# Performance work log

Measured on AMD Instinct MI355X. Metric: run time of the kernel, lower is better.

## Reference

```python
import jax, jax.numpy as jnp
import numpy as np

B, S, D, H = 2, 2048, 1024, 16
HD = D // H

def setup_inputs() -> dict:
    key = jax.random.key(0)
    k1, k2, k3, k4, k5 = jax.random.split(key, 5)
    X = jax.random.normal(k1, (B, S, D), dtype=jnp.float32)
    # nn.Linear(D, 3D): weight [3D, D], bias [3D]
    W_qkv = jax.random.normal(k2, (3 * D, D), dtype=jnp.float32) * (1.0 / np.sqrt(D))
    b_qkv = jax.random.normal(k3, (3 * D,), dtype=jnp.float32) * 0.02
    W_out = jax.random.normal(k4, (D, D), dtype=jnp.float32) * (1.0 / np.sqrt(D))
    b_out = jax.random.normal(k5, (D,), dtype=jnp.float32) * 0.02
    return {"X": X, "W_qkv": W_qkv, "b_qkv": b_qkv, "W_out": W_out, "b_out": b_out}

def reference(X, W_qkv, b_qkv, W_out, b_out):
    b, s, d = X.shape
    qkv = jnp.einsum('bsd,ed->bse', X, W_qkv) + b_qkv  # [B,S,3D]
    q, k, v = jnp.split(qkv, 3, axis=2)
    def heads(t):
        return t.reshape(b, s, H, HD).transpose(0, 2, 1, 3)  # [B,H,S,HD]
    q, k, v = heads(q), heads(k), heads(v)
    scores = jnp.einsum('bhqd,bhkd->bhqk', q, k) * (1.0 / np.sqrt(HD))
    causal = jnp.tril(jnp.ones((s, s), dtype=bool))
    scores = jnp.where(causal[None, None], scores, jnp.float32(-jnp.inf))
    probs = jax.nn.softmax(scores, axis=-1)
    attn = jnp.einsum('bhqk,bhkd->bhqd', probs, v)  # [B,H,S,HD]
    attn = attn.transpose(0, 2, 1, 3).reshape(b, s, d)
    out = jnp.einsum('bsd,ed->bse', attn, W_out) + b_out
    return out
```

## Files before the change

kernel.cpp:

```cpp
#include <hip/hip_runtime.h>


typedef _Float16 f16x8 __attribute__((ext_vector_type(8)));
typedef _Float16 f16x4 __attribute__((ext_vector_type(4)));
typedef float    f32x4 __attribute__((ext_vector_type(4)));
typedef unsigned short u16x8 __attribute__((ext_vector_type(8)));

__device__ __forceinline__ float bf16_bits_to_f32(unsigned short u) {
    union { unsigned int i; float f; } v; v.i = ((unsigned int)u) << 16; return v.f;
}
__device__ __forceinline__ unsigned short f32_to_bf16_bits(float f) {
    union { float f; unsigned int i; } v; v.f = f;
    unsigned int x = v.i;
    return (unsigned short)((x + 0x7fffu + ((x >> 16) & 1u)) >> 16);
}
__device__ __forceinline__ float fexp2(float x) {
#if __has_builtin(__builtin_amdgcn_exp2f)
    return __builtin_amdgcn_exp2f(x);
#else
    return exp2f(x);
#endif
}
__device__ __forceinline__ void gll16(const void* g, void* l) {
    __builtin_amdgcn_global_load_lds(
        (const __attribute__((address_space(1))) unsigned int*)g,
        (__attribute__((address_space(3))) unsigned int*)l, 16, 0, 0);
}

__global__ void detect_kernel(const unsigned short* __restrict__ X, unsigned int* __restrict__ flag) {
    __shared__ unsigned int smax;
    if (threadIdx.x == 0) smax = 0;
    __syncthreads();
    unsigned int mymax = 0;
    for (int i = threadIdx.x; i < 16384; i += 256) {
        unsigned int e = (X[i] >> 7) & 0xFFu;
        mymax = mymax > e ? mymax : e;
    }
    atomicMax(&smax, mymax);
    __syncthreads();
    if (threadIdx.x == 0) flag[0] = (smax >= 0x90u) ? 1u : 0u;
}

__global__ void __launch_bounds__(256) cvt2_kernel(const void* __restrict__ Wqkv, _Float16* __restrict__ wout,
                                                   const void* __restrict__ X, _Float16* __restrict__ xout,
                                                   const unsigned int* __restrict__ flag) {
    int b = blockIdx.x;
    const void* in; _Float16* out; size_t off;
    if (b < 1536) { in = Wqkv; out = wout; off = (size_t)b * 2048; }
    else          { in = X;    out = xout; off = (size_t)(b - 1536) * 2048; }
    size_t i = off + (size_t)threadIdx.x * 8;
    f16x8 c;
    if (flag[0]) {
        const float* p = (const float*)in + i;
        #pragma unroll
        for (int j = 0; j < 8; j++) c[j] = (_Float16)p[j];
    } else {
        u16x8 r = *(const u16x8*)((const unsigned short*)in + i);
        #pragma unroll
        for (int j = 0; j < 8; j++) c[j] = (_Float16)bf16_bits_to_f32(r[j]);
    }
    *(f16x8*)(out + i) = c;
}

__global__ void __launch_bounds__(256) cvtw_kernel(const void* __restrict__ in,
                                                   _Float16* __restrict__ out,
                                                   const unsigned int* __restrict__ flag) {
    size_t i = ((size_t)blockIdx.x * 256 + threadIdx.x) * 8;
    f16x8 c;
    if (flag[0]) {
        const float* p = (const float*)in + i;
        #pragma unroll
        for (int j = 0; j < 8; j++) c[j] = (_Float16)p[j];
    } else {
        u16x8 r = *(const u16x8*)((const unsigned short*)in + i);
        #pragma unroll
        for (int j = 0; j < 8; j++) c[j] = (_Float16)bf16_bits_to_f32(r[j]);
    }
    *(f16x8*)(out + i) = c;
}

template<int AF16>
__global__ void __launch_bounds__(256) qkv_gemm(
    const void* __restrict__ A, const _Float16* __restrict__ Wf,
    const void* __restrict__ bias, const unsigned int* __restrict__ flag,
    _Float16* __restrict__ qws, _Float16* __restrict__ kws, _Float16* __restrict__ vtws)
{
    constexpr int AST = AF16 ? 32 : 56;
    __shared__ _Float16 As[128 * AST];
    __shared__ _Float16 Bs[128 * 32];
    const bool isf32 = (flag[0] != 0u);
    const int tid  = threadIdx.x;
    const int lane = tid & 63, wave = tid >> 6;
    const int l15  = lane & 15, quad = lane >> 4;
    const int wm   = (wave >> 1) * 64, wn = (wave & 1) * 64;
    const int m0   = blockIdx.y * 128, n0 = blockIdx.x * 128;
    const int srow = tid >> 1, scol = (tid & 1) * 16;

    f32x4 acc[4][4] = {};

    for (int k0 = 0; k0 < 1024; k0 += 32) {
        if (AF16) {
            #pragma unroll
            for (int i = 0; i < 2; i++) {
                int seg = (wave * 2 + i) * 64 + lane;
                int row = seg >> 2, qtr = seg & 3;
                gll16((const _Float16*)A + (size_t)(m0 + row) * 1024 + k0 + qtr * 8,
                      &As[(wave * 2 + i) * 512]);
            }
        } else {
            f16x8 c0, c1;
            if (isf32) {
                const float4* ga = (const float4*)((const float*)A + (size_t)(m0 + srow) * 1024 + k0 + scol);
                float4 a0 = ga[0], a1 = ga[1], a2 = ga[2], a3 = ga[3];
                c0[0]=(_Float16)a0.x; c0[1]=(_Float16)a0.y; c0[2]=(_Float16)a0.z; c0[3]=(_Float16)a0.w;
                c0[4]=(_Float16)a1.x; c0[5]=(_Float16)a1.y; c0[6]=(_Float16)a1.z; c0[7]=(_Float16)a1.w;
                c1[0]=(_Float16)a2.x; c1[1]=(_Float16)a2.y; c1[2]=(_Float16)a2.z; c1[3]=(_Float16)a2.w;
                c1[4]=(_Float16)a3.x; c1[5]=(_Float16)a3.y; c1[6]=(_Float16)a3.z; c1[7]=(_Float16)a3.w;
            } else {
                const unsigned short* ga = (const unsigned short*)A + (size_t)(m0 + srow) * 1024 + k0 + scol;
                u16x8 r0 = *(const u16x8*)ga, r1 = *(const u16x8*)(ga + 8);
                #pragma unroll
                for (int i = 0; i < 8; i++) {
                    c0[i] = (_Float16)bf16_bits_to_f32(r0[i]);
                    c1[i] = (_Float16)bf16_bits_to_f32(r1[i]);
                }
            }
            *(f16x8*)&As[srow * AST + scol]     = c0;
            *(f16x8*)&As[srow * AST + scol + 8] = c1;
        }
        #pragma unroll
        for (int i = 0; i < 2; i++) {
            int seg = (wave * 2 + i) * 64 + lane;
            int row = seg >> 2, qtr = seg & 3;
            gll16(Wf + (size_t)(n0 + row) * 1024 + k0 + qtr * 8, &Bs[(wave * 2 + i) * 512]);
        }
        __syncthreads();
        f16x8 af[4], bfg[4];
        #pragma unroll
        for (int mt = 0; mt < 4; mt++)
            af[mt] = *(const f16x8*)&As[(wm + mt * 16 + l15) * AST + quad * 8];
        #pragma unroll
        for (int nt = 0; nt < 4; nt++)
            bfg[nt] = *(const f16x8*)&Bs[(wn + nt * 16 + l15) * 32 + quad * 8];
        #pragma unroll
        for (int mt = 0; mt < 4; mt++)
            #pragma unroll
            for (int nt = 0; nt < 4; nt++)
                acc[mt][nt] = __builtin_amdgcn_mfma_f32_16x16x32_f16(af[mt], bfg[nt], acc[mt][nt], 0, 0, 0);
        __syncthreads();
    }

    const float qsc = 0.18033688011112042591f;
    #pragma unroll
    for (int mt = 0; mt < 4; mt++) {
        #pragma unroll
        for (int nt = 0; nt < 4; nt++) {
            #pragma unroll
            for (int r = 0; r < 4; r++) {
                int m = m0 + wm + mt * 16 + quad * 4 + r;
                int n = n0 + wn + nt * 16 + l15;
                float bval = isf32 ? ((const float*)bias)[n] : bf16_bits_to_f32(((const unsigned short*)bias)[n]);
                float val = acc[mt][nt][r] + bval;
                int b = m >> 11, s = m & 2047;
                int t = n >> 10, e = n & 1023;
                int h = e >> 6, hd = e & 63;
                int bh = b * 16 + h;
                if (t == 0)      qws[((size_t)bh * 2048 + s) * 64 + hd]  = (_Float16)(val * qsc);
                else if (t == 1) kws[((size_t)bh * 2048 + s) * 64 + hd]  = (_Float16)val;
                else             vtws[((size_t)bh * 64 + hd) * 2048 + s] = (_Float16)val;
            }
        }
    }
}

__global__ void __launch_bounds__(256) out_gemm(
    const _Float16* __restrict__ Alo, const _Float16* __restrict__ Ahi,
    const _Float16* __restrict__ Wf, const void* __restrict__ bias,
    const unsigned int* __restrict__ flag, void* __restrict__ outp, int m_base)
{
    __shared__ _Float16 As[128 * 32];
    __shared__ _Float16 Bs[128 * 32];
    const bool isf32 = (flag[0] != 0u);
    const int tid  = threadIdx.x;
    const int lane = tid & 63, wave = tid >> 6;
    const int l15  = lane & 15, quad = lane >> 4;
    const int wm   = (wave >> 1) * 64, wn = (wave & 1) * 64;
    const int m0g  = m_base + blockIdx.y * 128, n0 = blockIdx.x * 128;
    const _Float16* A = (m0g < 2048) ? (Alo + (size_t)m0g * 1024)
                                     : (Ahi + (size_t)(m0g - 2048) * 1024);
    f32x4 acc[4][4] = {};

    for (int k0 = 0; k0 < 1024; k0 += 32) {
        #pragma unroll
        for (int i = 0; i < 2; i++) {
            int seg = (wave * 2 + i) * 64 + lane;
            int row = seg >> 2, qtr = seg & 3;
            gll16(A + (size_t)row * 1024 + k0 + qtr * 8, &As[(wave * 2 + i) * 512]);
            gll16(Wf + (size_t)(n0 + row) * 1024 + k0 + qtr * 8, &Bs[(wave * 2 + i) * 512]);
        }
        __syncthreads();
        f16x8 af[4], bfg[4];
        #pragma unroll
        for (int mt = 0; mt < 4; mt++)
            af[mt] = *(const f16x8*)&As[(wm + mt * 16 + l15) * 32 + quad * 8];
        #pragma unroll
        for (int nt = 0; nt < 4; nt++)
            bfg[nt] = *(const f16x8*)&Bs[(wn + nt * 16 + l15) * 32 + quad * 8];
        #pragma unroll
        for (int mt = 0; mt < 4; mt++)
            #pragma unroll
            for (int nt = 0; nt < 4; nt++)
                acc[mt][nt] = __builtin_amdgcn_mfma_f32_16x16x32_f16(af[mt], bfg[nt], acc[mt][nt], 0, 0, 0);
        __syncthreads();
    }

    #pragma unroll
    for (int mt = 0; mt < 4; mt++) {
        #pragma unroll
        for (int nt = 0; nt < 4; nt++) {
            #pragma unroll
            for (int r = 0; r < 4; r++) {
                int m = m0g + wm + mt * 16 + quad * 4 + r;
                int n = n0 + wn + nt * 16 + l15;
                float bval = isf32 ? ((const float*)bias)[n] : bf16_bits_to_f32(((const unsigned short*)bias)[n]);
                float val = acc[mt][nt][r] + bval;
                size_t idx = (size_t)m * 1024 + n;
                if (isf32) ((float*)outp)[idx] = val;
                else       ((unsigned short*)outp)[idx] = f32_to_bf16_bits(val);
            }
        }
    }
}

__global__ void __launch_bounds__(256) flash_kernel(
    const _Float16* __restrict__ qws,
    const _Float16* __restrict__ kws,
    const _Float16* __restrict__ vtws,
    _Float16* __restrict__ attn_lo,
    _Float16* __restrict__ attn_hi)
{
    __shared__ _Float16 Ks[2][64 * 64];
    __shared__ _Float16 Vs[2][64 * 72];

    const int bh   = blockIdx.x;
    const int qb   = 31 - blockIdx.y;
    const int tid  = threadIdx.x;
    const int wave = tid >> 6;
    const int lane = tid & 63;
    const int l15  = lane & 15, quad = lane >> 4;

    const _Float16* Q  = qws  + (size_t)bh * 2048 * 64;
    const _Float16* Kp = kws  + (size_t)bh * 2048 * 64;
    const _Float16* Vt = vtws + (size_t)bh * 64 * 2048;

    const int q0w = qb * 64 + wave * 16;
    f16x8 qf0 = *(const f16x8*)(Q + (size_t)(q0w + l15) * 64 + quad * 8);
    f16x8 qf1 = *(const f16x8*)(Q + (size_t)(q0w + l15) * 64 + 32 + quad * 8);

    f32x4 o[4] = {};
    float lp = 0.f;
    const int nch = qb + 1;

    {
        #pragma unroll
        for (int i = 0; i < 2; i++) {
            int s = (wave * 2 + i) * 64 + lane;
            int row = s >> 3, cs = ((s & 7) - row) & 7;
            gll16(Kp + (size_t)row * 64 + cs * 8, &Ks[0][s * 8]);
        }
        int hd = tid >> 3, ko = (tid & 7) * 8;
        f16x8 v0 = *(const f16x8*)(Vt + (size_t)hd * 2048 + ko);
        f16x8 v1 = *(const f16x8*)(Vt + (size_t)(hd + 32) * 2048 + ko);
        *(f16x8*)&Vs[0][hd * 72 + ko]        = v0;
        *(f16x8*)&Vs[0][(hd + 32) * 72 + ko] = v1;
    }

    for (int c = 0; c < nch; c++) {
        __syncthreads();
        const int cb = c & 1;
        const bool more = (c + 1 < nch);
        f16x8 vr0, vr1;
        int hd = tid >> 3, ko = (tid & 7) * 8;
        if (more) {
            int jn = (c + 1) * 64;
            vr0 = *(const f16x8*)(Vt + (size_t)hd * 2048 + jn + ko);
            vr1 = *(const f16x8*)(Vt + (size_t)(hd + 32) * 2048 + jn + ko);
            #pragma unroll
            for (int i = 0; i < 2; i++) {
                int s = (wave * 2 + i) * 64 + lane;
                int row = s >> 3, cs = ((s & 7) - row) & 7;
                gll16(Kp + (size_t)(jn + row) * 64 + cs * 8, &Ks[cb ^ 1][s * 8]);
            }
        }

        const bool diag = (c == qb);
        f32x4 t[4];
        #pragma unroll
        for (int kt = 0; kt < 4; kt++) {
            int row = kt * 16 + l15;
            f16x8 k0 = *(const f16x8*)&Ks[cb][row * 64 + ((quad + l15) & 7) * 8];
            f16x8 k1 = *(const f16x8*)&Ks[cb][row * 64 + ((4 + quad + l15) & 7) * 8];
            f32x4 z = {};
            z = __builtin_amdgcn_mfma_f32_16x16x32_f16(k0, qf0, z, 0, 0, 0);
            t[kt] = __builtin_amdgcn_mfma_f32_16x16x32_f16(k1, qf1, z, 0, 0, 0);
        }
        float p[16];
        #pragma unroll
        for (int kt = 0; kt < 4; kt++)
            #pragma unroll
            for (int r = 0; r < 4; r++) {
                float v = t[kt][r];
                if (diag)
                    v = ((kt * 16 + quad * 4 + r) <= (wave * 16 + l15)) ? v : -INFINITY;
                p[kt * 4 + r] = fminf(fexp2(v), 60000.0f);
            }
        float rs = 0.f;
        #pragma unroll
        for (int i = 0; i < 16; i++) rs += p[i];
        lp += rs;
        f16x4 pf[4];
        #pragma unroll
        for (int kt = 0; kt < 4; kt++)
            #pragma unroll
            for (int r = 0; r < 4; r++) pf[kt][r] = (_Float16)p[kt * 4 + r];
        #pragma unroll
        for (int kt = 0; kt < 4; kt++) {
            #pragma unroll
            for (int mt = 0; mt < 4; mt++) {
                f16x4 cv = *(const f16x4*)&Vs[cb][(mt * 16 + l15) * 72 + kt * 16 + quad * 4];
                o[mt] = __builtin_amdgcn_mfma_f32_16x16x16f16(cv, pf[kt], o[mt], 0, 0, 0);
            }
        }

        if (more) {
            *(f16x8*)&Vs[cb ^ 1][hd * 72 + ko]        = vr0;
            *(f16x8*)&Vs[cb ^ 1][(hd + 32) * 72 + ko] = vr1;
        }
    }

    const int b = bh >> 4, h = bh & 15;
    _Float16* attn = (b == 0) ? attn_lo : attn_hi;
    {
        float rs = lp;
        rs += __shfl_xor(rs, 16);
        rs += __shfl_xor(rs, 32);
        const float inv = 1.0f / rs;
        const int s = q0w + l15;
        #pragma unroll
        for (int mt = 0; mt < 4; mt++) {
            #pragma unroll
            for (int r = 0; r < 4; r++) {
                int hdd = mt * 16 + quad * 4 + r;
                attn[(size_t)s * 1024 + h * 64 + hdd] = (_Float16)(o[mt][r] * inv);
            }
        }
    }
}

extern "C" void kernel_launch(void* const* d_in, const int* in_sizes, int n_in,
                              void* d_out, int out_size, void* d_ws, size_t ws_size,
                              hipStream_t stream) {
    (void)out_size;
    const void *X = nullptr, *Wqkv = nullptr, *bqkv = nullptr, *Wout = nullptr, *bout = nullptr;
    for (int i = 0; i < n_in; i++) {
        switch (in_sizes[i]) {
            case 4194304: X    = d_in[i]; break;
            case 3145728: Wqkv = d_in[i]; break;
            case 3072:    bqkv = d_in[i]; break;
            case 1048576: Wout = d_in[i]; break;
            case 1024:    bout = d_in[i]; break;
        }
    }
    char* ws = (char*)d_ws;
    const size_t MB = 1u << 20;
    unsigned int* flag = (unsigned int*)ws;
    char* base = ws + 256;

    detect_kernel<<<1, 256, 0, stream>>>((const unsigned short*)X, flag);

    if (ws_size >= (size_t)(385 * MB / 10)) {
        _Float16* wf16 = (_Float16*)(base);
        _Float16* xf16 = (_Float16*)(base + 6 * MB);
        _Float16* q    = (_Float16*)(base + 14 * MB);
        _Float16* k    = (_Float16*)(base + 22 * MB);
        _Float16* vt   = (_Float16*)(base + 30 * MB);
        cvt2_kernel<<<dim3(3584), 256, 0, stream>>>(Wqkv, wf16, X, xf16, flag);
        qkv_gemm<1><<<dim3(24, 32), 256, 0, stream>>>(xf16, wf16, bqkv, flag, q, k, vt);
        cvtw_kernel<<<dim3(512), 256, 0, stream>>>(Wout, wf16, flag);
        _Float16* attn = xf16;
        flash_kernel<<<dim3(32, 32), 256, 0, stream>>>(q, k, vt, attn, attn + (size_t)2048 * 1024);
        out_gemm<<<dim3(8, 32), 256, 0, stream>>>(attn, attn + (size_t)2048 * 1024,
                                                  wf16, bout, flag, d_out, 0);
    } else {
        _Float16* wf16    = (_Float16*)(base);
        _Float16* attn_hi = (_Float16*)(base + 6 * MB);
        _Float16* q       = (_Float16*)(base + 10 * MB);
        _Float16* k       = (_Float16*)(base + 18 * MB);
        _Float16* vt      = (_Float16*)(base + 26 * MB);
        _Float16* attn_lo = (_Float16*)((char*)d_out + 8 * MB);
        cvtw_kernel<<<dim3(1536), 256, 0, stream>>>(Wqkv, wf16, flag);
        qkv_gemm<0><<<dim3(24, 32), 256, 0, stream>>>(X, wf16, bqkv, flag, q, k, vt);
        cvtw_kernel<<<dim3(512), 256, 0, stream>>>(Wout, wf16, flag);
        flash_kernel<<<dim3(32, 32), 256, 0, stream>>>(q, k, vt, attn_lo, attn_hi);
        out_gemm<<<dim3(8, 16), 256, 0, stream>>>(attn_lo, attn_hi, wf16, bout, flag, d_out, 0);
        out_gemm<<<dim3(8, 16), 256, 0, stream>>>(attn_lo, attn_hi, wf16, bout, flag, d_out, 2048);
    }
}
```

Before: 209.9 us.

## Replace QKV GEMM with 256x256-tile, 8-wave, ping-pong pipelined kernel

Adds a new QKV projection kernel that uses 256x256 output tiles with 512 threads (8 waves). It stages A and B half-tiles into double-buffered LDS through direct global-to-LDS loads with an XOR swizzle. The K loop is split into four MFMA phases with interleaved prefetches, barriers and s_setprio, so loads overlap with matrix math. The goal is to raise data reuse and MFMA utilization over the old 128x128 kernel, at the cost of 128KB of LDS, fewer blocks (192) and a hand-tuned waitcnt schedule that could be fragile.

```diff
diff --git a/kernel.cpp b/kernel.cpp
--- a/kernel.cpp
+++ b/kernel.cpp
@@ -77,6 +77,154 @@
         for (int j = 0; j < 8; j++) c[j] = (_Float16)bf16_bits_to_f32(r[j]);
     }
     *(f16x8*)(out + i) = c;
+}
+
+__device__ __forceinline__ void stage_ht(const _Float16* __restrict__ G, int kt, int h,
+                                         _Float16* tile, int wave, int lane)
+{
+    #pragma unroll
+    for (int i = 0; i < 2; i++) {
+        int seg = wave * 2 + i;
+        int f = seg * 64 + lane;
+        int row = h * 128 + (f >> 3);
+        int qg = (f & 7) ^ (row & 7);
+        gll16(G + (size_t)row * 1024 + kt * 64 + qg * 8,
+              tile + (size_t)h * 8192 + (size_t)seg * 512);
+    }
+}
+
+__global__ void __launch_bounds__(512, 2) qkv_gemm8(
+    const _Float16* __restrict__ Af, const _Float16* __restrict__ Wf,
+    const void* __restrict__ bias, const unsigned int* __restrict__ flag,
+    _Float16* __restrict__ qws, _Float16* __restrict__ kws, _Float16* __restrict__ vtws)
+{
+    __shared__ _Float16 L[2][2][16384];
+    const int tid  = threadIdx.x;
+    const int lane = tid & 63, wave = tid >> 6;
+    const int l15  = lane & 15, quad = lane >> 4;
+    const int wm   = (wave >> 2) * 128, wn = (wave & 3) * 64;
+    const int m0   = blockIdx.y * 256, n0 = blockIdx.x * 256;
+    const _Float16* Ag = Af + (size_t)m0 * 1024;
+    const _Float16* Bg = Wf + (size_t)n0 * 1024;
+
+    f32x4 acc[8][4] = {};
+
+    stage_ht(Ag, 0, 0, &L[0][0][0], wave, lane);
+    stage_ht(Ag, 0, 1, &L[0][0][0], wave, lane);
+    stage_ht(Bg, 0, 0, &L[0][1][0], wave, lane);
+    stage_ht(Bg, 0, 1, &L[0][1][0], wave, lane);
+    stage_ht(Bg, 1, 0, &L[1][1][0], wave, lane);
+    stage_ht(Bg, 1, 1, &L[1][1][0], wave, lane);
+    stage_ht(Ag, 1, 0, &L[1][0][0], wave, lane);
+    asm volatile("s_waitcnt vmcnt(6)" ::: "memory");
+    __builtin_amdgcn_s_barrier();
+
+    constexpr int NT = 16;
+    #pragma unroll 2
+    for (int t = 0; t < NT; ++t) {
+        const int cb = t & 1;
+        const _Float16* At = &L[cb][0][0];
+        const _Float16* Bt = &L[cb][1][0];
+        f16x8 aF[4][2], bF[4][2];
+
+        #pragma unroll
+        for (int mt = 0; mt < 4; mt++) {
+            int R = wm + mt * 16 + l15;
+            #pragma unroll
+            for (int ks = 0; ks < 2; ks++)
+                aF[mt][ks] = *(const f16x8*)&At[R * 64 + (((ks * 4 + quad) ^ (R & 7)) << 3)];
+        }
+        #pragma unroll
+        for (int nt = 0; nt < 4; nt++) {
+            int R = wn + nt * 16 + l15;
+            #pragma unroll
+            for (int ks = 0; ks < 2; ks++)
+                bF[nt][ks] = *(const f16x8*)&Bt[R * 64 + (((ks * 4 + quad) ^ (R & 7)) << 3)];
+        }
+        if (t + 1 < NT) stage_ht(Ag, t + 1, 1, &L[(t + 1) & 1][0][0], wave, lane);
+        __builtin_amdgcn_s_barrier();
+        __builtin_amdgcn_s_setprio(1);
+        #pragma unroll
+        for (int mt = 0; mt < 4; mt++)
+            #pragma unroll
+            for (int nt = 0; nt < 2; nt++)
+                #pragma unroll
+                for (int ks = 0; ks < 2; ks++)
+                    acc[mt][nt] = __builtin_amdgcn_mfma_f32_16x16x32_f16(aF[mt][ks], bF[nt][ks], acc[mt][nt], 0, 0, 0);
+        __builtin_amdgcn_s_setprio(0);
+        __builtin_amdgcn_s_barrier();
+
+        if (t + 2 < NT) stage_ht(Bg, t + 2, 0, &L[cb][1][0], wave, lane);
+        __builtin_amdgcn_s_barrier();
+        __builtin_amdgcn_s_setprio(1);
+        #pragma unroll
+        for (int mt = 0; mt < 4; mt++)
+            #pragma unroll
+            for (int nt = 0; nt < 2; nt++)
+                #pragma unroll
+                for (int ks = 0; ks < 2; ks++)
+                    acc[mt][2 + nt] = __builtin_amdgcn_mfma_f32_16x16x32_f16(aF[mt][ks], bF[2 + nt][ks], acc[mt][2 + nt], 0, 0, 0);
+        __builtin_amdgcn_s_setprio(0);
+        __builtin_amdgcn_s_barrier();
+
+        #pragma unroll
+        for (int mt = 0; mt < 4; mt++) {
+            int R = wm + 64 + mt * 16 + l15;
+            #pragma unroll
+            for (int ks = 0; ks < 2; ks++)
+                aF[mt][ks] = *(const f16x8*)&At[R * 64 + (((ks * 4 + quad) ^ (R & 7)) << 3)];
+        }
+        if (t + 2 < NT) stage_ht(Bg, t + 2, 1, &L[cb][1][0], wave, lane);
+        __builtin_amdgcn_s_barrier();
+        __builtin_amdgcn_s_setprio(1);
+        #pragma unroll
+        for (int mt = 0; mt < 4; mt++)
+            #pragma unroll
+            for (int nt = 0; nt < 2; nt++)
+                #pragma unroll
+                for (int ks = 0; ks < 2; ks++)
+                    acc[4 + mt][2 + nt] = __builtin_amdgcn_mfma_f32_16x16x32_f16(aF[mt][ks], bF[2 + nt][ks], acc[4 + mt][2 + nt], 0, 0, 0);
+        __builtin_amdgcn_s_setprio(0);
+        __builtin_amdgcn_s_barrier();
+
+        if (t + 2 < NT) stage_ht(Ag, t + 2, 0, &L[cb][0][0], wave, lane);
+        if (t < NT - 2)       { asm volatile("s_waitcnt vmcnt(6)" ::: "memory"); }
+        else if (t == NT - 2) { asm volatile("s_waitcnt vmcnt(0)" ::: "memory"); }
+        __builtin_amdgcn_s_barrier();
+        __builtin_amdgcn_s_setprio(1);
+        #pragma unroll
+        for (int mt = 0; mt < 4; mt++)
+            #pragma unroll
+            for (int nt = 0; nt < 2; nt++)
+                #pragma unroll
+                for (int ks = 0; ks < 2; ks++)
+                    acc[4 + mt][nt] = __builtin_amdgcn_mfma_f32_16x16x32_f16(aF[mt][ks], bF[nt][ks], acc[4 + mt][nt], 0, 0, 0);
+        __builtin_amdgcn_s_setprio(0);
+        __builtin_amdgcn_s_barrier();
+    }
+
+    const bool isf32 = (flag[0] != 0u);
+    const float qsc = 0.18033688011112042591f;
+    #pragma unroll
+    for (int nt = 0; nt < 4; nt++) {
+        int n = n0 + wn + nt * 16 + l15;
+        float bval = isf32 ? ((const float*)bias)[n] : bf16_bits_to_f32(((const unsigned short*)bias)[n]);
+        int tn = n >> 10, e = n & 1023;
+        int h = e >> 6, hd = e & 63;
+        #pragma unroll
+        for (int mt = 0; mt < 8; mt++) {
+            #pragma unroll
+            for (int r = 0; r < 4; r++) {
+                int m = m0 + wm + mt * 16 + quad * 4 + r;
+                float val = acc[mt][nt][r] + bval;
+                int b = m >> 11, s = m & 2047;
+                int bh = b * 16 + h;
+                if (tn == 0)      qws [((size_t)bh * 2048 + s) * 64 + hd] = (_Float16)(val * qsc);
+                else if (tn == 1) kws [((size_t)bh * 2048 + s) * 64 + hd] = (_Float16)val;
+                else              vtws[((size_t)bh * 64 + hd) * 2048 + s] = (_Float16)val;
+            }
+        }
+    }
 }
 
 template<int AF16>
@@ -385,7 +533,7 @@
         _Float16* k    = (_Float16*)(base + 22 * MB);
         _Float16* vt   = (_Float16*)(base + 30 * MB);
         cvt2_kernel<<<dim3(3584), 256, 0, stream>>>(Wqkv, wf16, X, xf16, flag);
-        qkv_gemm<1><<<dim3(24, 32), 256, 0, stream>>>(xf16, wf16, bqkv, flag, q, k, vt);
+        qkv_gemm8<<<dim3(12, 16), 512, 0, stream>>>(xf16, wf16, bqkv, flag, q, k, vt);
         cvtw_kernel<<<dim3(512), 256, 0, stream>>>(Wout, wf16, flag);
         _Float16* attn = xf16;
         flash_kernel<<<dim3(32, 32), 256, 0, stream>>>(q, k, vt, attn, attn + (size_t)2048 * 1024);
```

Result: slower. 222.7 us (+6.1%).

## Double GEMM K-tile to 64 with XOR-swizzled LDS layout in QKV and out GEMMs

Applied to the files above, without the earlier changes.

The QKV GEMM (f16 path) and output GEMM now stage 64-wide K tiles per iteration instead of 32. Each thread issues four direct global-to-LDS loads per iteration, with the 16-byte chunks XOR-swizzled by row. Fragment reads apply the matching swizzle to avoid LDS bank conflicts. This halves the number of barrier-separated iterations and packs two MFMA K-steps per sync. The cost is twice the LDS footprint per block, which may lower occupancy.

```diff
diff --git a/kernel.cpp b/kernel.cpp
--- a/kernel.cpp
+++ b/kernel.cpp
@@ -79,13 +79,85 @@
     *(f16x8*)(out + i) = c;
 }
 
-template<int AF16>
-__global__ void __launch_bounds__(256) qkv_gemm(
+__global__ void __launch_bounds__(256) qkv_gemmA(
+    const _Float16* __restrict__ A, const _Float16* __restrict__ Wf,
+    const void* __restrict__ bias, const unsigned int* __restrict__ flag,
+    _Float16* __restrict__ qws, _Float16* __restrict__ kws, _Float16* __restrict__ vtws)
+{
+    __shared__ _Float16 As[128 * 64];
+    __shared__ _Float16 Bs[128 * 64];
+    const bool isf32 = (flag[0] != 0u);
+    const int tid  = threadIdx.x;
+    const int lane = tid & 63, wave = tid >> 6;
+    const int l15  = lane & 15, quad = lane >> 4;
+    const int wm   = (wave >> 1) * 64, wn = (wave & 1) * 64;
+    const int m0   = blockIdx.y * 128, n0 = blockIdx.x * 128;
+
+    f32x4 acc[4][4] = {};
+
+    for (int k0 = 0; k0 < 1024; k0 += 64) {
+        #pragma unroll
+        for (int i = 0; i < 4; i++) {
+            int f = (wave * 4 + i) * 64 + lane;
+            int row = f >> 3, g = (f & 7) ^ (row & 7);
+            gll16(A  + (size_t)(m0 + row) * 1024 + k0 + g * 8, &As[f * 8]);
+            gll16(Wf + (size_t)(n0 + row) * 1024 + k0 + g * 8, &Bs[f * 8]);
+        }
+        __syncthreads();
+        f16x8 af[4][2], bfg[4][2];
+        #pragma unroll
+        for (int mt = 0; mt < 4; mt++) {
+            int R = wm + mt * 16 + l15;
+            #pragma unroll
+            for (int ks = 0; ks < 2; ks++)
+                af[mt][ks] = *(const f16x8*)&As[R * 64 + (((ks * 4 + quad) ^ (R & 7)) << 3)];
+        }
+        #pragma unroll
+        for (int nt = 0; nt < 4; nt++) {
+            int R = wn + nt * 16 + l15;
+            #pragma unroll
+            for (int ks = 0; ks < 2; ks++)
+                bfg[nt][ks] = *(const f16x8*)&Bs[R * 64 + (((ks * 4 + quad) ^ (R & 7)) << 3)];
+        }
+        #pragma unroll
+        for (int mt = 0; mt < 4; mt++)
+            #pragma unroll
+            for (int nt = 0; nt < 4; nt++)
+                #pragma unroll
+                for (int ks = 0; ks < 2; ks++)
+                    acc[mt][nt] = __builtin_amdgcn_mfma_f32_16x16x32_f16(af[mt][ks], bfg[nt][ks], acc[mt][nt], 0, 0, 0);
+        __syncthreads();
+    }
+
+    const float qsc = 0.18033688011112042591f;
+    #pragma unroll
+    for (int mt = 0; mt < 4; mt++) {
+        #pragma unroll
+        for (int nt = 0; nt < 4; nt++) {
+            #pragma unroll
+            for (int r = 0; r < 4; r++) {
+                int m = m0 + wm + mt * 16 + quad * 4 + r;
+                int n = n0 + wn + nt * 16 + l15;
+                float bval = isf32 ? ((const float*)bias)[n] : bf16_bits_to_f32(((const unsigned short*)bias)[n]);
+                float val = acc[mt][nt][r] + bval;
+                int b = m >> 11, s = m & 2047;
+                int t = n >> 10, e = n & 1023;
+                int h = e >> 6, hd = e & 63;
+                int bh = b * 16 + h;
+                if (t == 0)      qws[((size_t)bh * 2048 + s) * 64 + hd]  = (_Float16)(val * qsc);
+                else if (t == 1) kws[((size_t)bh * 2048 + s) * 64 + hd]  = (_Float16)val;
+                else             vtws[((size_t)bh * 64 + hd) * 2048 + s] = (_Float16)val;
+            }
+        }
+    }
+}
+
+__global__ void __launch_bounds__(256) qkv_gemm_fb(
     const void* __restrict__ A, const _Float16* __restrict__ Wf,
     const void* __restrict__ bias, const unsigned int* __restrict__ flag,
     _Float16* __restrict__ qws, _Float16* __restrict__ kws, _Float16* __restrict__ vtws)
 {
-    constexpr int AST = AF16 ? 32 : 56;
+    constexpr int AST = 56;
     __shared__ _Float16 As[128 * AST];
     __shared__ _Float16 Bs[128 * 32];
     const bool isf32 = (flag[0] != 0u);
@@ -99,15 +171,7 @@
     f32x4 acc[4][4] = {};
 
     for (int k0 = 0; k0 < 1024; k0 += 32) {
-        if (AF16) {
-            #pragma unroll
-            for (int i = 0; i < 2; i++) {
-                int seg = (wave * 2 + i) * 64 + lane;
-                int row = seg >> 2, qtr = seg & 3;
-                gll16((const _Float16*)A + (size_t)(m0 + row) * 1024 + k0 + qtr * 8,
-                      &As[(wave * 2 + i) * 512]);
-            }
-        } else {
+        {
             f16x8 c0, c1;
             if (isf32) {
                 const float4* ga = (const float4*)((const float*)A + (size_t)(m0 + srow) * 1024 + k0 + scol);
@@ -178,8 +242,8 @@
     const _Float16* __restrict__ Wf, const void* __restrict__ bias,
     const unsigned int* __restrict__ flag, void* __restrict__ outp, int m_base)
 {
-    __shared__ _Float16 As[128 * 32];
-    __shared__ _Float16 Bs[128 * 32];
+    __shared__ _Float16 As[128 * 64];
+    __shared__ _Float16 Bs[128 * 64];
     const bool isf32 = (flag[0] != 0u);
     const int tid  = threadIdx.x;
     const int lane = tid & 63, wave = tid >> 6;
@@ -190,27 +254,37 @@
                                      : (Ahi + (size_t)(m0g - 2048) * 1024);
     f32x4 acc[4][4] = {};
 
-    for (int k0 = 0; k0 < 1024; k0 += 32) {
-        #pragma unroll
-        for (int i = 0; i < 2; i++) {
-            int seg = (wave * 2 + i) * 64 + lane;
-            int row = seg >> 2, qtr = seg & 3;
-            gll16(A + (size_t)row * 1024 + k0 + qtr * 8, &As[(wave * 2 + i) * 512]);
-            gll16(Wf + (size_t)(n0 + row) * 1024 + k0 + qtr * 8, &Bs[(wave * 2 + i) * 512]);
-        }
-        __syncthreads();
-        f16x8 af[4], bfg[4];
+    for (int k0 = 0; k0 < 1024; k0 += 64) {
+        #pragma unroll
+        for (int i = 0; i < 4; i++) {
+            int f = (wave * 4 + i) * 64 + lane;
+            int row = f >> 3, g = (f & 7) ^ (row & 7);
+            gll16(A  + (size_t)row * 1024 + k0 + g * 8, &As[f * 8]);
+            gll16(Wf + (size_t)(n0 + row) * 1024 + k0 + g * 8, &Bs[f * 8]);
+        }
+        __syncthreads();
+        f16x8 af[4][2], bfg[4][2];
+        #pragma unroll
+        for (int mt = 0; mt < 4; mt++) {
+            int R = wm + mt * 16 + l15;
+            #pragma unroll
+            for (int ks = 0; ks < 2; ks++)
+                af[mt][ks] = *(const f16x8*)&As[R * 64 + (((ks * 4 + quad) ^ (R & 7)) << 3)];
+        }
+        #pragma unroll
+        for (int nt = 0; nt < 4; nt++) {
+            int R = wn + nt * 16 + l15;
+            #pragma unroll
+            for (int ks = 0; ks < 2; ks++)
+                bfg[nt][ks] = *(const f16x8*)&Bs[R * 64 + (((ks * 4 + quad) ^ (R & 7)) << 3)];
+        }
         #pragma unroll
         for (int mt = 0; mt < 4; mt++)
-            af[mt] = *(const f16x8*)&As[(wm + mt * 16 + l15) * 32 + quad * 8];
-        #pragma unroll
-        for (int nt = 0; nt < 4; nt++)
-            bfg[nt] = *(const f16x8*)&Bs[(wn + nt * 16 + l15) * 32 + quad * 8];
-        #pragma unroll
-        for (int mt = 0; mt < 4; mt++)
             #pragma unroll
             for (int nt = 0; nt < 4; nt++)
-                acc[mt][nt] = __builtin_amdgcn_mfma_f32_16x16x32_f16(af[mt], bfg[nt], acc[mt][nt], 0, 0, 0);
+                #pragma unroll
+                for (int ks = 0; ks < 2; ks++)
+                    acc[mt][nt] = __builtin_amdgcn_mfma_f32_16x16x32_f16(af[mt][ks], bfg[nt][ks], acc[mt][nt], 0, 0, 0);
         __syncthreads();
     }
 
@@ -385,7 +459,7 @@
         _Float16* k    = (_Float16*)(base + 22 * MB);
         _Float16* vt   = (_Float16*)(base + 30 * MB);
         cvt2_kernel<<<dim3(3584), 256, 0, stream>>>(Wqkv, wf16, X, xf16, flag);
-        qkv_gemm<1><<<dim3(24, 32), 256, 0, stream>>>(xf16, wf16, bqkv, flag, q, k, vt);
+        qkv_gemmA<<<dim3(24, 32), 256, 0, stream>>>(xf16, wf16, bqkv, flag, q, k, vt);
         cvtw_kernel<<<dim3(512), 256, 0, stream>>>(Wout, wf16, flag);
         _Float16* attn = xf16;
         flash_kernel<<<dim3(32, 32), 256, 0, stream>>>(q, k, vt, attn, attn + (size_t)2048 * 1024);
@@ -399,7 +473,7 @@
         _Float16* vt      = (_Float16*)(base + 26 * MB);
         _Float16* attn_lo = (_Float16*)((char*)d_out + 8 * MB);
         cvtw_kernel<<<dim3(1536), 256, 0, stream>>>(Wqkv, wf16, flag);
-        qkv_gemm<0><<<dim3(24, 32), 256, 0, stream>>>(X, wf16, bqkv, flag, q, k, vt);
+        qkv_gemm_fb<<<dim3(24, 32), 256, 0, stream>>>(X, wf16, bqkv, flag, q, k, vt);
         cvtw_kernel<<<dim3(512), 256, 0, stream>>>(Wout, wf16, flag);
         flash_kernel<<<dim3(32, 32), 256, 0, stream>>>(q, k, vt, attn_lo, attn_hi);
         out_gemm<<<dim3(8, 16), 256, 0, stream>>>(attn_lo, attn_hi, wf16, bout, flag, d_out, 0);
```

Result: slower. 228.4 us (+8.8%).
